# Performance work log

Measured on AMD Instinct MI355X. Metric: run time of the kernel, lower is better.

Reference implementation:

```python
import jax, jax.numpy as jnp
import numpy as np

H = 768      # hidden_size (MambaConfig default)
DI = 500     # intermediate_size (overridden)
N = 16       # state_size
R = 48       # time_step_rank = ceil(768/16)
K = 4        # conv_kernel
LYR = 5      # num_hidden_layers
EPS = 1e-5   # layer_norm_epsilon
B, L, IN = 8, 1024, 4096


def _rmsnorm(x, w):
    v = jnp.mean(jnp.square(x), axis=-1, keepdims=True)
    return x * jax.lax.rsqrt(v + EPS) * w


def _mixer(x, in_proj, conv_w, conv_b, x_proj, dt_w, dt_b, A_log, Dp, out_w):
    # x: [B, L, H]
    proj = x @ in_proj                       # [B, L, 2*DI]
    u, gate = jnp.split(proj, 2, axis=-1)
    # causal depthwise conv1d (torch Conv1d padding=K-1, sliced to L)
    up = jnp.pad(u, ((0, 0), (K - 1, 0), (0, 0)))
    conv = conv_b
    for k in range(K):
        conv = conv + up[:, k:k + x.shape[1], :] * conv_w[:, k]
    u = jax.nn.silu(conv)                    # [B, L, DI]
    ssm = u @ x_proj                         # [B, L, R + 2N]
    dt, Bm, Cm = ssm[..., :R], ssm[..., R:R + N], ssm[..., R + N:]
    dt = jax.nn.softplus(dt @ dt_w + dt_b)   # [B, L, DI]
    A = -jnp.exp(A_log)                      # [DI, N]
    dA = jnp.exp(dt[..., None] * A)          # [B, L, DI, N]
    dBu = dt[..., None] * Bm[:, :, None, :] * u[..., None]  # [B, L, DI, N]

    def step(h, xs):
        dA_t, dBu_t, C_t = xs
        h = dA_t * h + dBu_t                 # [B, DI, N]
        y = jnp.einsum('bdn,bn->bd', h, C_t)
        return h, y

    h0 = jnp.zeros((u.shape[0], DI, N), dtype=u.dtype)
    _, ys = jax.lax.scan(step, h0, (dA.transpose(1, 0, 2, 3),
                                    dBu.transpose(1, 0, 2, 3),
                                    Cm.transpose(1, 0, 2)))
    y = ys.transpose(1, 0, 2)                # [B, L, DI]
    y = y + u * Dp
    y = y * jax.nn.silu(gate)
    return y @ out_w                         # [B, L, H]


def setup_inputs() -> dict:
    key = jax.random.key(0)
    ks = jax.random.split(key, 12)
    s = 0.02
    inputs = jax.random.normal(ks[0], (B, L, IN), jnp.float32)
    W_down = jax.random.normal(ks[1], (IN, H), jnp.float32) * s
    in_proj = jax.random.normal(ks[2], (LYR, H, 2 * DI), jnp.float32) * s
    conv_w = jax.random.normal(ks[3], (LYR, DI, K), jnp.float32) * 0.1
    conv_b = jnp.zeros((LYR, DI), jnp.float32)
    x_proj = jax.random.normal(ks[4], (LYR, DI, R + 2 * N), jnp.float32) * s
    dt_w = jax.random.normal(ks[5], (LYR, R, DI), jnp.float32) * s
    dt_b = jax.random.normal(ks[6], (LYR, DI), jnp.float32) * 0.1
    A_log = jnp.broadcast_to(jnp.log(jnp.arange(1, N + 1, dtype=jnp.float32)),
                             (LYR, DI, N)).copy()
    D_param = jnp.ones((LYR, DI), jnp.float32)
    out_w = jax.random.normal(ks[7], (LYR, DI, H), jnp.float32) * s
    norm_w = jnp.ones((LYR, H), jnp.float32)
    norm_f_w = jnp.ones((H,), jnp.float32)
    W_cls = jax.random.normal(ks[8], (H, 1), jnp.float32) * s
    return dict(inputs=inputs, W_down=W_down, in_proj=in_proj, conv_w=conv_w,
                conv_b=conv_b, x_proj=x_proj, dt_w=dt_w, dt_b=dt_b,
                A_log=A_log, D_param=D_param, out_w=out_w, norm_w=norm_w,
                norm_f_w=norm_f_w, W_cls=W_cls)


def reference(inputs, W_down, in_proj, conv_w, conv_b, x_proj, dt_w, dt_b,
              A_log, D_param, out_w, norm_w, norm_f_w, W_cls):
    x = inputs @ W_down                      # down projection [B, L, H]
    for i in range(LYR):
        x = x + _mixer(_rmsnorm(x, norm_w[i]), in_proj[i], conv_w[i],
                       conv_b[i], x_proj[i], dt_w[i], dt_b[i], A_log[i],
                       D_param[i], out_w[i])
    x = _rmsnorm(x, norm_f_w)
    out = x[:, -1]                           # last token [B, H]
    logits = out @ W_cls                     # [B, 1]
    return logits
```

## Files before the change

kernel.cpp:

```cpp
#include <hip/hip_runtime.h>
#include <hip/hip_bf16.h>

#define BATCH 8
#define SEQL 1024
#define INDIM 4096
#define HDIM 768
#define DI 500
#define NSTATE 16
#define RRANK 48
#define KCONV 4
#define NLAYER 5
#define BL (BATCH * SEQL)

typedef __attribute__((ext_vector_type(8))) short bf16x8;
typedef __attribute__((ext_vector_type(4))) float f32x4;

__device__ __forceinline__ void gl_lds16(const void* g, void* l) {
  __builtin_amdgcn_global_load_lds(
      (const __attribute__((address_space(1))) void*)g,
      (__attribute__((address_space(3))) void*)l, 16, 0, 0);
}

__device__ __forceinline__ unsigned short f2bf(float v) {
  return __hip_bfloat16_raw(__float2bfloat16(v)).x;
}
__device__ __forceinline__ float bf2f(unsigned short h) {
  unsigned int u = ((unsigned int)h) << 16;
  float f;
  memcpy(&f, &u, 4);
  return f;
}

template <int EPI>
__global__ __launch_bounds__(256) void gemm_mfma(
    const short* __restrict__ A, const short* __restrict__ Bt,
    float* __restrict__ C, const float* __restrict__ bias,
    unsigned short* __restrict__ D0, unsigned short* __restrict__ D1,
    int M, int N, int K, int lda, int ldb, int ldc) {
  __shared__ short As[128 * 32];
  __shared__ short Bs[128 * 32];
  const int tid = threadIdx.x;
  const int w = tid >> 6, lane = tid & 63;
  const int m0 = blockIdx.y * 128, n0 = blockIdx.x * 128;
  const int wr = w >> 1, wc = w & 1;
  f32x4 acc[4][4] = {};

  const int srow = tid >> 2;
  const int scol = (tid & 3) * 8;
  const short* ga0 = A + (size_t)(m0 + srow) * lda + scol;
  const short* ga1 = A + (size_t)(m0 + 64 + srow) * lda + scol;
  const short* gb0 = Bt + (size_t)(n0 + srow) * ldb + scol;
  const short* gb1 = Bt + (size_t)(n0 + 64 + srow) * ldb + scol;
  short* lA0 = As + w * 512;
  short* lA1 = As + 2048 + w * 512;
  short* lB0 = Bs + w * 512;
  short* lB1 = Bs + 2048 + w * 512;
  const int lr = lane & 15, kb = lane >> 4;

  for (int k0 = 0; k0 < K; k0 += 32) {
    gl_lds16(ga0, lA0);
    gl_lds16(ga1, lA1);
    gl_lds16(gb0, lB0);
    gl_lds16(gb1, lB1);
    ga0 += 32; ga1 += 32; gb0 += 32; gb1 += 32;
    __syncthreads();
    bf16x8 af[4], bfr[4];
#pragma unroll
    for (int i = 0; i < 4; ++i) {
      af[i] = *(const bf16x8*)(As + (wr * 64 + i * 16 + lr) * 32 + kb * 8);
      bfr[i] = *(const bf16x8*)(Bs + (wc * 64 + i * 16 + lr) * 32 + kb * 8);
    }
#pragma unroll
    for (int i = 0; i < 4; ++i)
#pragma unroll
      for (int j = 0; j < 4; ++j)
        acc[i][j] = __builtin_amdgcn_mfma_f32_16x16x32_bf16(af[i], bfr[j],
                                                            acc[i][j], 0, 0, 0);
    __syncthreads();
  }

#pragma unroll
  for (int i = 0; i < 4; ++i) {
    const int row = m0 + wr * 64 + i * 16 + (lane >> 4) * 4;
#pragma unroll
    for (int j = 0; j < 4; ++j) {
      const int col = n0 + wc * 64 + j * 16 + (lane & 15);
      if (col < N) {
        if (EPI == 3) {
          float4 v4;
#pragma unroll
          for (int r = 0; r < 4; ++r) {
            float v = acc[i][j][r] + bias[col];
            ((float*)&v4)[r] = (v > 15.f) ? v : log1pf(expf(v));
          }
          const int bb = row >> 10, tt = row & 1023;
          *(float4*)&C[((size_t)bb * DI + col) * 1024 + tt] = v4;
        } else if (EPI == 4) {
#pragma unroll
          for (int r = 0; r < 4; ++r) {
            unsigned short h = f2bf(acc[i][j][r]);
            size_t rr = (size_t)(row + r);
            if (col < DI)
              D0[rr * 512 + col] = h;
            else
              D1[rr * 512 + (col - DI)] = h;
          }
        } else {
#pragma unroll
          for (int r = 0; r < 4; ++r) {
            float v = acc[i][j][r];
            size_t idx = (size_t)(row + r) * ldc + col;
            if (EPI == 1) v += C[idx];
            if (EPI == 2) {
              v += bias[col];
              v = (v > 15.f) ? v : log1pf(expf(v));
            }
            C[idx] = v;
          }
        }
      }
    }
  }
}

__global__ __launch_bounds__(256) void convert_cast(
    const float* __restrict__ src, __hip_bfloat16* __restrict__ dst, long n) {
  long i = ((long)blockIdx.x * 256 + threadIdx.x) * 4;
  if (i >= n) return;
  float4 v = *(const float4*)(src + i);
  dst[i + 0] = __float2bfloat16(v.x);
  dst[i + 1] = __float2bfloat16(v.y);
  dst[i + 2] = __float2bfloat16(v.z);
  dst[i + 3] = __float2bfloat16(v.w);
}

__global__ __launch_bounds__(256) void convert_wT(
    const float* __restrict__ src, __hip_bfloat16* __restrict__ dst, int K,
    int N, int Kpad, int Npad, long src_lstride, long dst_lstride) {
  int idx = blockIdx.x * 256 + threadIdx.x;
  int per = Kpad * Npad;
  if (idx >= per) return;
  const float* s = src + (long)blockIdx.y * src_lstride;
  __hip_bfloat16* d = dst + (long)blockIdx.y * dst_lstride;
  int n = idx / Kpad, k = idx % Kpad;
  float v = (k < K && n < N) ? s[(long)k * N + n] : 0.f;
  d[idx] = __float2bfloat16(v);
}

__device__ __forceinline__ float block_sum256(float v, float* sm) {
#pragma unroll
  for (int off = 32; off > 0; off >>= 1) v += __shfl_down(v, off, 64);
  int wid = threadIdx.x >> 6;
  if ((threadIdx.x & 63) == 0) sm[wid] = v;
  __syncthreads();
  float t = sm[0] + sm[1] + sm[2] + sm[3];
  __syncthreads();
  return t;
}

__global__ __launch_bounds__(256) void rmsnorm_kernel(
    const float* __restrict__ X, const float* __restrict__ w,
    __hip_bfloat16* __restrict__ XN) {
  __shared__ float sm[4];
  const long row = blockIdx.x;
  const float* x = X + row * HDIM;
  float vals[3];
  float s = 0.f;
#pragma unroll
  for (int j = 0; j < 3; ++j) {
    vals[j] = x[threadIdx.x + j * 256];
    s += vals[j] * vals[j];
  }
  float tot = block_sum256(s, sm);
  float scale = rsqrtf(tot / (float)HDIM + 1e-5f);
#pragma unroll
  for (int j = 0; j < 3; ++j) {
    int c = threadIdx.x + j * 256;
    XN[row * HDIM + c] = __float2bfloat16(vals[j] * scale * w[c]);
  }
}

__global__ __launch_bounds__(256) void conv_fused_kernel(
    const unsigned short* __restrict__ Uraw, const float* __restrict__ cw,
    const float* __restrict__ cb, unsigned short* __restrict__ Ubf,
    unsigned short* __restrict__ Ut, int layer) {
  __shared__ unsigned short tin[35][33];
  __shared__ unsigned short tout[32][33];
  const int d0 = blockIdx.x * 32, t0 = blockIdx.y * 32, b = blockIdx.z;
  const int tx = threadIdx.x & 31, ty = threadIdx.x >> 5;
#pragma unroll
  for (int r = 0; r < 5; ++r) {
    int tr = ty + r * 8;
    if (tr < 35) {
      int t = t0 + tr - (KCONV - 1);
      tin[tr][tx] =
          (t >= 0) ? Uraw[((size_t)b * 1024 + t) * 512 + d0 + tx] : 0;
    }
  }
  __syncthreads();
  const int d = d0 + tx;
  float w0 = 0.f, w1 = 0.f, w2 = 0.f, w3 = 0.f, bias = 0.f;
  if (d < DI) {
    const float* w = cw + ((size_t)layer * DI + d) * KCONV;
    w0 = w[0]; w1 = w[1]; w2 = w[2]; w3 = w[3];
    bias = cb[layer * DI + d];
  }
#pragma unroll
  for (int r = 0; r < 4; ++r) {
    const int tt = ty + r * 8;
    unsigned short h = 0;
    if (d < DI) {
      float a = bias + w0 * bf2f(tin[tt][tx]) + w1 * bf2f(tin[tt + 1][tx]) +
                w2 * bf2f(tin[tt + 2][tx]) + w3 * bf2f(tin[tt + 3][tx]);
      h = f2bf(a / (1.f + expf(-a)));
    }
    tout[tt][tx] = h;
    Ubf[((size_t)b * 1024 + t0 + tt) * 512 + d] = h;
  }
  __syncthreads();
#pragma unroll
  for (int r = 0; r < 4; ++r) {
    const int dd = ty + r * 8;
    Ut[((size_t)b * 512 + d0 + dd) * 1024 + t0 + tx] = tout[tx][dd];
  }
}

__global__ __launch_bounds__(256) void dtconv_kernel(
    const float* __restrict__ SSM, __hip_bfloat16* __restrict__ SSMbf) {
  long idx = (long)blockIdx.x * 256 + threadIdx.x;
  if (idx >= (long)BL * 64) return;
  int c = (int)(idx & 63);
  long row = idx >> 6;
  float v = (c < RRANK) ? SSM[row * 128 + c] : 0.f;
  SSMbf[idx] = __float2bfloat16(v);
}

__global__ __launch_bounds__(256) void y_gate_kernel(
    const unsigned short* __restrict__ Yt, const unsigned short* __restrict__ G,
    unsigned short* __restrict__ Ybf) {
  __shared__ unsigned short tile[32][33];
  const int d0 = blockIdx.x * 32, t0 = blockIdx.y * 32, b = blockIdx.z;
  const int tx = threadIdx.x & 31, ty = threadIdx.x >> 5;
#pragma unroll
  for (int r = 0; r < 4; ++r) {
    int d = d0 + ty + r * 8;
    tile[ty + r * 8][tx] =
        (d < DI) ? Yt[((size_t)b * 512 + d) * 1024 + t0 + tx]
                 : (unsigned short)0;
  }
  __syncthreads();
#pragma unroll
  for (int r = 0; r < 4; ++r) {
    size_t row = (size_t)b * 1024 + t0 + ty + r * 8;
    int d = d0 + tx;
    float yv = 0.f;
    if (d < DI) {
      float y = bf2f(tile[tx][ty + r * 8]);
      float g = bf2f(G[row * 512 + d]);
      yv = y * (g / (1.f + expf(-g)));
    }
    Ybf[row * 512 + d] = f2bf(yv);
  }
}

__global__ __launch_bounds__(256) void scan_kernel(
    const float* __restrict__ DTt, const unsigned short* __restrict__ Ut,
    const float* __restrict__ SSM, const float* __restrict__ A_log,
    const float* __restrict__ Dparam, unsigned short* __restrict__ Yt,
    int layer) {
  __shared__ float sdt[1040];
  __shared__ float su[1040];
  __shared__ float s_ap[16][17];
  __shared__ float s_h0[16][17];
  __shared__ float s_hi[16][17];
  const int blk = blockIdx.x;
  const int b = blk / DI, d = blk % DI;
  const int tid = threadIdx.x;
  const int c = tid >> 4, n = tid & 15;

  const float* dtp = DTt + ((size_t)b * DI + d) * 1024;
  const unsigned short* up = Ut + ((size_t)b * 512 + d) * 1024;
#pragma unroll
  for (int k = 0; k < 4; ++k) {
    int x = tid + k * 256;
    sdt[x + (x >> 6)] = dtp[x];
    su[x + (x >> 6)] = bf2f(up[x]);
  }
  __syncthreads();

  const float An = -expf(A_log[((size_t)layer * DI + d) * NSTATE + n]);
  const float Dp = Dparam[layer * DI + d];
  const int t0 = c * 64;
  const int sb = t0 + c;
  const float* ssmB = SSM + ((size_t)b * 1024 + t0) * 128 + RRANK + n;

  float h = 0.f, ap = 1.f;
  for (int s = 0; s < 64; ++s) {
    float dt = sdt[sb + s];
    float a = __expf(dt * An);
    h = a * h + dt * su[sb + s] * ssmB[(size_t)s * 128];
    ap *= a;
  }
  s_ap[c][n] = ap;
  s_h0[c][n] = h;
  __syncthreads();

  if (tid < 16) {
    float hi = 0.f;
    for (int cc = 0; cc < 16; ++cc) {
      s_hi[cc][tid] = hi;
      hi = s_ap[cc][tid] * hi + s_h0[cc][tid];
    }
  }
  __syncthreads();

  h = s_hi[c][n];
  unsigned short* yp = Yt + ((size_t)b * 512 + d) * 1024 + t0;
  for (int s = 0; s < 64; ++s) {
    float dt = sdt[sb + s];
    float u = su[sb + s];
    float a = __expf(dt * An);
    h = a * h + dt * u * ssmB[(size_t)s * 128];
    float p = h * ssmB[(size_t)s * 128 + 16];
    p += __shfl_xor(p, 1, 64);
    p += __shfl_xor(p, 2, 64);
    p += __shfl_xor(p, 4, 64);
    p += __shfl_xor(p, 8, 64);
    if (n == 0) {
      float y = p + u * Dp;
      yp[s] = f2bf(y);
    }
  }
}

__global__ __launch_bounds__(256) void final_kernel(
    const float* __restrict__ X, const float* __restrict__ nfw,
    const float* __restrict__ Wcls, float* __restrict__ out) {
  __shared__ float sm[4];
  const int b = blockIdx.x;
  const long row = (long)b * SEQL + (SEQL - 1);
  const float* x = X + row * HDIM;
  float vals[3];
  float s = 0.f;
#pragma unroll
  for (int j = 0; j < 3; ++j) {
    vals[j] = x[threadIdx.x + j * 256];
    s += vals[j] * vals[j];
  }
  float tot = block_sum256(s, sm);
  float scale = rsqrtf(tot / (float)HDIM + 1e-5f);
  float dot = 0.f;
#pragma unroll
  for (int j = 0; j < 3; ++j) {
    int c = threadIdx.x + j * 256;
    dot += vals[j] * scale * nfw[c] * Wcls[c];
  }
  float td = block_sum256(dot, sm);
  if (threadIdx.x == 0) out[b] = td;
}

extern "C" void kernel_launch(void* const* d_in, const int* in_sizes, int n_in,
                              void* d_out, int out_size, void* d_ws,
                              size_t ws_size, hipStream_t stream) {
  const float* inputs  = (const float*)d_in[0];
  const float* W_down  = (const float*)d_in[1];
  const float* in_proj = (const float*)d_in[2];
  const float* conv_w  = (const float*)d_in[3];
  const float* conv_b  = (const float*)d_in[4];
  const float* x_proj  = (const float*)d_in[5];
  const float* dt_w    = (const float*)d_in[6];
  const float* dt_b    = (const float*)d_in[7];
  const float* A_log   = (const float*)d_in[8];
  const float* D_param = (const float*)d_in[9];
  const float* out_w   = (const float*)d_in[10];
  const float* norm_w  = (const float*)d_in[11];
  const float* norm_fw = (const float*)d_in[12];
  const float* W_cls   = (const float*)d_in[13];
  float* out = (float*)d_out;

  char* ws = (char*)d_ws;
  __hip_bfloat16* Abf   = (__hip_bfloat16*)(ws + 0);
  __hip_bfloat16* Wdbf  = (__hip_bfloat16*)(ws + 67108864);
  __hip_bfloat16* XNbf  = (__hip_bfloat16*)(ws + 0);
  unsigned short* Yt    = (unsigned short*)(ws + 0);
  float*          DTt   = (float*)(ws + 12582912);
  unsigned short* Uraw  = (unsigned short*)(ws + 28966912);
  unsigned short* Ybf   = (unsigned short*)(ws + 28966912);
  unsigned short* Gate  = (unsigned short*)(ws + 37355520);
  unsigned short* Ubf   = (unsigned short*)(ws + 45744128);
  unsigned short* Ut    = (unsigned short*)(ws + 54132736);
  float*          SSM   = (float*)(ws + 62521344);
  __hip_bfloat16* SSMbf = (__hip_bfloat16*)(ws + 66715648);
  float*          X     = (float*)(ws + 73400320);
  __hip_bfloat16* inpbf = (__hip_bfloat16*)(ws + 98566144);
  __hip_bfloat16* xpbf  = (__hip_bfloat16*)(ws + 106430464);
  __hip_bfloat16* dtwbf = (__hip_bfloat16*)(ws + 107085824);
  __hip_bfloat16* outwbf= (__hip_bfloat16*)(ws + 107413504);

  convert_cast<<<(long)BL * 4096 / 4 / 256, 256, 0, stream>>>(inputs, Abf,
                                                              (long)BL * 4096);
  convert_wT<<<dim3((768 * 4096 + 255) / 256, 1), 256, 0, stream>>>(
      W_down, Wdbf, 4096, 768, 4096, 768, 0, 0);
  convert_wT<<<dim3((768 * 1024 + 255) / 256, NLAYER), 256, 0, stream>>>(
      in_proj, inpbf, 768, 1000, 768, 1024, (long)HDIM * 1000, 768 * 1024);
  convert_wT<<<dim3((128 * 512 + 255) / 256, NLAYER), 256, 0, stream>>>(
      x_proj, xpbf, 500, 80, 512, 128, (long)DI * 80, 128 * 512);
  convert_wT<<<dim3((512 * 64 + 255) / 256, NLAYER), 256, 0, stream>>>(
      dt_w, dtwbf, 48, 500, 64, 512, (long)RRANK * DI, 512 * 64);
  convert_wT<<<dim3((768 * 512 + 255) / 256, NLAYER), 256, 0, stream>>>(
      out_w, outwbf, 500, 768, 512, 768, (long)DI * HDIM, 768 * 512);

  gemm_mfma<0><<<dim3(768 / 128, BL / 128), 256, 0, stream>>>(
      (const short*)Abf, (const short*)Wdbf, X, nullptr, nullptr, nullptr, BL,
      HDIM, INDIM, INDIM, INDIM, HDIM);

  for (int i = 0; i < NLAYER; ++i) {
    rmsnorm_kernel<<<BL, 256, 0, stream>>>(X, norm_w + i * HDIM, XNbf);
    gemm_mfma<4><<<dim3(1024 / 128, BL / 128), 256, 0, stream>>>(
        (const short*)XNbf, (const short*)(inpbf + (long)i * 768 * 1024),
        nullptr, nullptr, Uraw, Gate, BL, 1000, HDIM, HDIM, HDIM, 0);
    conv_fused_kernel<<<dim3(16, 32, 8), 256, 0, stream>>>(Uraw, conv_w,
                                                           conv_b, Ubf, Ut, i);
    gemm_mfma<0><<<dim3(1, BL / 128), 256, 0, stream>>>(
        (const short*)Ubf, (const short*)(xpbf + (long)i * 128 * 512), SSM,
        nullptr, nullptr, nullptr, BL, 80, 512, 512, 512, 128);
    dtconv_kernel<<<(long)BL * 64 / 256, 256, 0, stream>>>(SSM, SSMbf);
    gemm_mfma<3><<<dim3(512 / 128, BL / 128), 256, 0, stream>>>(
        (const short*)SSMbf, (const short*)(dtwbf + (long)i * 512 * 64), DTt,
        dt_b + i * DI, nullptr, nullptr, BL, DI, 64, 64, 64, 0);
    scan_kernel<<<BATCH * DI, 256, 0, stream>>>(DTt, Ut, SSM, A_log, D_param,
                                                Yt, i);
    y_gate_kernel<<<dim3(16, 32, 8), 256, 0, stream>>>(Yt, Gate, Ybf);
    gemm_mfma<1><<<dim3(768 / 128, BL / 128), 256, 0, stream>>>(
        (const short*)Ybf, (const short*)(outwbf + (long)i * 768 * 512), X,
        nullptr, nullptr, nullptr, BL, HDIM, 512, 512, 512, HDIM);
  }

  final_kernel<<<BATCH, 256, 0, stream>>>(X, norm_fw, W_cls, out);
}
```

Before: 1.272 ms.

## Double-buffer GEMM LDS tiles, XOR-swizzle layout, fuse dt bf16 cast into x_proj GEMM

The MFMA GEMM now uses two LDS buffers, so the global-to-LDS load for the next K-slice is issued before computing the current one, and it drops one barrier per iteration. LDS columns are XOR-swizzled by row to reduce bank conflicts on the bf16x8 fragment reads. A new epilogue (EPI 5) writes the x_proj result in fp32 and also emits the zero-padded bf16 dt slice, which removes the separate dtconv kernel launch. Doubling shared memory per block may lower occupancy.

```diff
diff --git a/kernel.cpp b/kernel.cpp
--- a/kernel.cpp
+++ b/kernel.cpp
@@ -37,8 +37,8 @@
     float* __restrict__ C, const float* __restrict__ bias,
     unsigned short* __restrict__ D0, unsigned short* __restrict__ D1,
     int M, int N, int K, int lda, int ldb, int ldc) {
-  __shared__ short As[128 * 32];
-  __shared__ short Bs[128 * 32];
+  __shared__ short As[2][128 * 32];
+  __shared__ short Bs[2][128 * 32];
   const int tid = threadIdx.x;
   const int w = tid >> 6, lane = tid & 63;
   const int m0 = blockIdx.y * 128, n0 = blockIdx.x * 128;
@@ -46,29 +46,27 @@
   f32x4 acc[4][4] = {};
 
   const int srow = tid >> 2;
-  const int scol = (tid & 3) * 8;
-  const short* ga0 = A + (size_t)(m0 + srow) * lda + scol;
-  const short* ga1 = A + (size_t)(m0 + 64 + srow) * lda + scol;
-  const short* gb0 = Bt + (size_t)(n0 + srow) * ldb + scol;
-  const short* gb1 = Bt + (size_t)(n0 + 64 + srow) * ldb + scol;
-  short* lA0 = As + w * 512;
-  short* lA1 = As + 2048 + w * 512;
-  short* lB0 = Bs + w * 512;
-  short* lB1 = Bs + 2048 + w * 512;
+  const int cpos = tid & 3;
+  const int sc = (cpos ^ ((srow >> 1) & 3)) * 8;
+  const short* ga0 = A + (size_t)(m0 + srow) * lda + sc;
+  const short* ga1 = A + (size_t)(m0 + 64 + srow) * lda + sc;
+  const short* gb0 = Bt + (size_t)(n0 + srow) * ldb + sc;
+  const short* gb1 = Bt + (size_t)(n0 + 64 + srow) * ldb + sc;
   const int lr = lane & 15, kb = lane >> 4;
-
-  for (int k0 = 0; k0 < K; k0 += 32) {
-    gl_lds16(ga0, lA0);
-    gl_lds16(ga1, lA1);
-    gl_lds16(gb0, lB0);
-    gl_lds16(gb1, lB1);
-    ga0 += 32; ga1 += 32; gb0 += 32; gb1 += 32;
-    __syncthreads();
+  const int kbx = (kb ^ ((lr >> 1) & 3)) * 8;
+
+  auto stage = [&](int buf, int k0) {
+    gl_lds16(ga0 + k0, &As[buf][w * 512]);
+    gl_lds16(ga1 + k0, &As[buf][2048 + w * 512]);
+    gl_lds16(gb0 + k0, &Bs[buf][w * 512]);
+    gl_lds16(gb1 + k0, &Bs[buf][2048 + w * 512]);
+  };
+  auto compute = [&](int buf) {
     bf16x8 af[4], bfr[4];
 #pragma unroll
     for (int i = 0; i < 4; ++i) {
-      af[i] = *(const bf16x8*)(As + (wr * 64 + i * 16 + lr) * 32 + kb * 8);
-      bfr[i] = *(const bf16x8*)(Bs + (wc * 64 + i * 16 + lr) * 32 + kb * 8);
+      af[i] = *(const bf16x8*)&As[buf][(wr * 64 + i * 16 + lr) * 32 + kbx];
+      bfr[i] = *(const bf16x8*)&Bs[buf][(wc * 64 + i * 16 + lr) * 32 + kbx];
     }
 #pragma unroll
     for (int i = 0; i < 4; ++i)
@@ -76,8 +74,19 @@
       for (int j = 0; j < 4; ++j)
         acc[i][j] = __builtin_amdgcn_mfma_f32_16x16x32_bf16(af[i], bfr[j],
                                                             acc[i][j], 0, 0, 0);
+  };
+
+  const int nk = K >> 5;
+  stage(0, 0);
+  __syncthreads();
+  int cur = 0;
+  for (int t = 0; t < nk - 1; ++t) {
+    stage(cur ^ 1, (t + 1) * 32);
+    compute(cur);
     __syncthreads();
-  }
+    cur ^= 1;
+  }
+  compute(cur);
 
 #pragma unroll
   for (int i = 0; i < 4; ++i) {
@@ -85,8 +94,8 @@
 #pragma unroll
     for (int j = 0; j < 4; ++j) {
       const int col = n0 + wc * 64 + j * 16 + (lane & 15);
-      if (col < N) {
-        if (EPI == 3) {
+      if (EPI == 3) {
+        if (col < N) {
           float4 v4;
 #pragma unroll
           for (int r = 0; r < 4; ++r) {
@@ -95,26 +104,32 @@
           }
           const int bb = row >> 10, tt = row & 1023;
           *(float4*)&C[((size_t)bb * DI + col) * 1024 + tt] = v4;
-        } else if (EPI == 4) {
-#pragma unroll
-          for (int r = 0; r < 4; ++r) {
-            unsigned short h = f2bf(acc[i][j][r]);
-            size_t rr = (size_t)(row + r);
-            if (col < DI)
-              D0[rr * 512 + col] = h;
-            else
-              D1[rr * 512 + (col - DI)] = h;
-          }
-        } else {
+        }
+      } else if (EPI == 4) {
+#pragma unroll
+        for (int r = 0; r < 4; ++r) {
+          unsigned short h = f2bf(acc[i][j][r]);
+          size_t rr = (size_t)(row + r);
+          if (col < DI)
+            D0[rr * 512 + col] = h;
+          else
+            D1[rr * 512 + (col - DI)] = h;
+        }
+      } else if (EPI == 5) {
+#pragma unroll
+        for (int r = 0; r < 4; ++r) {
+          float v = acc[i][j][r];
+          size_t rr = (size_t)(row + r);
+          if (col < N) C[rr * ldc + col] = v;
+          if (col < 64) D0[rr * 64 + col] = f2bf(col < RRANK ? v : 0.f);
+        }
+      } else {
+        if (col < N) {
 #pragma unroll
           for (int r = 0; r < 4; ++r) {
             float v = acc[i][j][r];
             size_t idx = (size_t)(row + r) * ldc + col;
             if (EPI == 1) v += C[idx];
-            if (EPI == 2) {
-              v += bias[col];
-              v = (v > 15.f) ? v : log1pf(expf(v));
-            }
             C[idx] = v;
           }
         }
@@ -223,16 +238,6 @@
     const int dd = ty + r * 8;
     Ut[((size_t)b * 512 + d0 + dd) * 1024 + t0 + tx] = tout[tx][dd];
   }
-}
-
-__global__ __launch_bounds__(256) void dtconv_kernel(
-    const float* __restrict__ SSM, __hip_bfloat16* __restrict__ SSMbf) {
-  long idx = (long)blockIdx.x * 256 + threadIdx.x;
-  if (idx >= (long)BL * 64) return;
-  int c = (int)(idx & 63);
-  long row = idx >> 6;
-  float v = (c < RRANK) ? SSM[row * 128 + c] : 0.f;
-  SSMbf[idx] = __float2bfloat16(v);
 }
 
 __global__ __launch_bounds__(256) void y_gate_kernel(
@@ -421,10 +426,9 @@
         nullptr, nullptr, Uraw, Gate, BL, 1000, HDIM, HDIM, HDIM, 0);
     conv_fused_kernel<<<dim3(16, 32, 8), 256, 0, stream>>>(Uraw, conv_w,
                                                            conv_b, Ubf, Ut, i);
-    gemm_mfma<0><<<dim3(1, BL / 128), 256, 0, stream>>>(
+    gemm_mfma<5><<<dim3(1, BL / 128), 256, 0, stream>>>(
         (const short*)Ubf, (const short*)(xpbf + (long)i * 128 * 512), SSM,
-        nullptr, nullptr, nullptr, BL, 80, 512, 512, 512, 128);
-    dtconv_kernel<<<(long)BL * 64 / 256, 256, 0, stream>>>(SSM, SSMbf);
+        nullptr, (unsigned short*)SSMbf, nullptr, BL, 80, 512, 512, 512, 128);
     gemm_mfma<3><<<dim3(512 / 128, BL / 128), 256, 0, stream>>>(
         (const short*)SSMbf, (const short*)(dtwbf + (long)i * 512 * 64), DTt,
         dt_b + i * DI, nullptr, nullptr, BL, DI, 64, 64, 64, 0);
```

Measured after the change: 1.265 ms. Within noise of the previous version (-0.5%).
